# Performance work log

Hardware: AMD Instinct MI355X
Metric: run time of the kernel (lower is better)

Reference implementation:

```python
import jax, jax.numpy as jnp
import numpy as np

B, S, D_IN, D_OUT = 4, 2048, 1024, 64
USE_MASK = True

def setup_inputs() -> dict:
    key = jax.random.key(0)
    ks = jax.random.split(key, 6)
    return {
        "inputs_for_keys": jax.random.normal(ks[0], (B, S, D_IN), jnp.float32),
        "inputs_for_values": jax.random.normal(ks[1], (B, S, D_IN), jnp.float32),
        "inputs_for_queries": jax.random.normal(ks[2], (B, S, D_IN), jnp.float32),
        "Weight_Q": jax.random.normal(ks[3], (D_IN, D_OUT), jnp.float32) * 0.02,
        "Weight_K": jax.random.normal(ks[4], (D_IN, D_OUT), jnp.float32) * 0.02,
        "Weight_V": jax.random.normal(ks[5], (D_IN, D_OUT), jnp.float32) * 0.02,
    }

def reference(inputs_for_keys, inputs_for_values, inputs_for_queries, Weight_Q, Weight_K, Weight_V):
    Q = jnp.einsum('bsd,de->bse', inputs_for_queries, Weight_Q)
    K = jnp.einsum('bsd,de->bse', inputs_for_keys, Weight_K)
    V = jnp.einsum('bsd,de->bse', inputs_for_values, Weight_V)
    # scores: [B, S_q, S_k], scaled by sqrt(d_out)
    scores = jnp.einsum('bqe,bke->bqk', Q, K) / np.sqrt(D_OUT).astype(np.float32)
    if USE_MASK:
        # -inf strictly above the diagonal (causal mask), matching
        # transpose(tril(ones*-inf, -1)) in the original.
        q_idx = jnp.arange(S)[:, None]
        k_idx = jnp.arange(S)[None, :]
        scores = jnp.where(k_idx > q_idx, -jnp.inf, scores)
    attn = jax.nn.softmax(scores, axis=-1)
    return jnp.einsum('bqk,bke->bqe', attn, V)
```

## Files before the change

### kernel.cpp

```cpp
#include <hip/hip_runtime.h>
#include <hip/hip_bf16.h>
#include <stdint.h>

typedef __bf16 bf16_t;
typedef __bf16 bf16x8 __attribute__((ext_vector_type(8)));
typedef float f32x4 __attribute__((ext_vector_type(4)));

#define L2E 1.44269504088896340736f

static __device__ __forceinline__ f32x4 mfma16(bf16x8 a, bf16x8 b, f32x4 c) {
  return __builtin_amdgcn_mfma_f32_16x16x32_bf16(a, b, c, 0, 0, 0);
}

static __device__ __forceinline__ void gload_lds16(const void* g, void* l) {
  __builtin_amdgcn_global_load_lds(
      (const __attribute__((address_space(1))) uint32_t*)g,
      (__attribute__((address_space(3))) uint32_t*)l, 16, 0, 0);
}

__global__ __launch_bounds__(256) void wt_kernel(const float* __restrict__ Wq,
                                                 const float* __restrict__ Wk,
                                                 const float* __restrict__ Wv,
                                                 bf16_t* __restrict__ Wt) {
  int gid = blockIdx.x * 256 + threadIdx.x;
  int proj = gid >> 16;
  int rem = gid & 65535;
  int k = rem >> 6, n = rem & 63;
  const float* W = (proj == 0) ? Wq : (proj == 1) ? Wk : Wv;
  float v = W[rem];
  if (proj == 0) v *= 0.125f;
  Wt[proj * 65536 + n * 1024 + k] = (bf16_t)v;
}

__global__ __launch_bounds__(128) void proj_kernel(
    const float* __restrict__ Xq, const float* __restrict__ Xk, const float* __restrict__ Xv,
    const bf16_t* __restrict__ Wt,
    bf16_t* __restrict__ Qb, bf16_t* __restrict__ Kb, bf16_t* __restrict__ Vt) {
  __shared__ alignas(16) char Wl[2][16384];
  __shared__ bf16_t Vb[2][16][68];

  int tid = threadIdx.x;
  int w = tid >> 6, lane = tid & 63;
  int l15 = lane & 15, g = lane >> 4;
  int bid = blockIdx.x;
  int p = bid >> 8, rt = bid & 255;
  int m0 = rt * 32;
  const float* X = (p == 0) ? Xq : (p == 1) ? Xk : Xv;
  const char* wbase = (const char*)(Wt + (size_t)p * 65536);

  int sn = w * 4 + (lane >> 4);
  int skb = (lane & 15) * 16;

  auto stageW = [&](int c, int buf) {
#pragma unroll
    for (int i = 0; i < 8; ++i) {
      int n = i * 8 + sn;
      const char* src = wbase + (size_t)n * 2048 + c * 256 + (skb ^ ((n & 7) << 4));
      gload_lds16(src, &Wl[buf][i * 2048 + w * 1024]);
    }
  };

  const float* xrow = X + (size_t)(m0 + w * 16 + l15) * 1024 + g * 8;

  auto issueX = [&](int c, float4* xr) {
    const float* b = xrow + c * 128;
#pragma unroll
    for (int j = 0; j < 4; ++j) {
      xr[2 * j] = *(const float4*)(b + j * 32);
      xr[2 * j + 1] = *(const float4*)(b + j * 32 + 4);
    }
  };

  f32x4 acc[4] = {};

  auto compute = [&](int c, const float4* xr) {
    const char* wb = &Wl[c & 1][0];
#pragma unroll
    for (int j = 0; j < 4; ++j) {
      bf16x8 af;
      af[0] = (bf16_t)xr[2 * j].x; af[1] = (bf16_t)xr[2 * j].y;
      af[2] = (bf16_t)xr[2 * j].z; af[3] = (bf16_t)xr[2 * j].w;
      af[4] = (bf16_t)xr[2 * j + 1].x; af[5] = (bf16_t)xr[2 * j + 1].y;
      af[6] = (bf16_t)xr[2 * j + 1].z; af[7] = (bf16_t)xr[2 * j + 1].w;
#pragma unroll
      for (int ct = 0; ct < 4; ++ct) {
        int n = ct * 16 + l15;
        bf16x8 bfr = *(const bf16x8*)(wb + n * 256 + ((j * 64 + g * 16) ^ ((n & 7) << 4)));
        acc[ct] = mfma16(af, bfr, acc[ct]);
      }
    }
  };

  float4 xA[8], xB[8];
  stageW(0, 0);
  issueX(0, xA);
#pragma unroll
  for (int c = 0; c < 8; ++c) {
    __syncthreads();
    if (c < 7) {
      stageW(c + 1, (c + 1) & 1);
      if (c & 1) issueX(c + 1, xA); else issueX(c + 1, xB);
    }
    if (c & 1) compute(c, xB); else compute(c, xA);
  }

  if (p < 2) {
    bf16_t* Ob = (p == 0) ? Qb : Kb;
    size_t rbase = (size_t)(m0 + w * 16 + g * 4) * 64 + l15;
#pragma unroll
    for (int ct = 0; ct < 4; ++ct)
#pragma unroll
      for (int r = 0; r < 4; ++r)
        Ob[rbase + (size_t)r * 64 + ct * 16] = (bf16_t)acc[ct][r];
  } else {
#pragma unroll
    for (int ct = 0; ct < 4; ++ct)
#pragma unroll
      for (int r = 0; r < 4; ++r)
        Vb[w][g * 4 + r][ct * 16 + l15] = (bf16_t)acc[ct][r];
    int d = lane;
    bf16_t tmp[16];
#pragma unroll
    for (int s = 0; s < 16; ++s) tmp[s] = Vb[w][s][d];
    int b = rt >> 6;
    int s0 = (m0 & 2047) + w * 16;
    bf16_t* dst = Vt + ((size_t)(b * 64 + d)) * 2048 + s0;
    *(uint4*)dst = *(const uint4*)&tmp[0];
    *(uint4*)(dst + 8) = *(const uint4*)&tmp[8];
  }
}

#define NW 8
__global__ __launch_bounds__(512) void attn_kernel(
    const bf16_t* __restrict__ Qb, const bf16_t* __restrict__ Kb,
    const bf16_t* __restrict__ Vt, float* __restrict__ Out) {
  __shared__ alignas(16) char Psm[NW * 4096];
  __shared__ float accL[NW][32][64];
  __shared__ float mL[NW][32];
  __shared__ float lL[NW][32];

  int b = blockIdx.y;
  int x = blockIdx.x;
  int qt = (b >= 2) ? (63 - x) : x;
  int q0 = qt * 32;
  int tid = threadIdx.x;
  int w = tid >> 6, lane = tid & 63;
  int l15 = lane & 15, g = lane >> 4;
  char* Pw = Psm + w * 4096;

  bf16x8 qf[2][2];
#pragma unroll
  for (int h = 0; h < 2; ++h) {
    size_t qrow = (size_t)(b * 2048 + q0 + h * 16 + l15) * 64;
    qf[h][0] = *(const bf16x8*)(Qb + qrow + g * 8);
    qf[h][1] = *(const bf16x8*)(Qb + qrow + 32 + g * 8);
  }

  float m_run[2][4], l_run[2][4];
  f32x4 acc_o[2][4] = {};
#pragma unroll
  for (int h = 0; h < 2; ++h)
#pragma unroll
    for (int r = 0; r < 4; ++r) { m_run[h][r] = -1e30f; l_run[h][r] = 0.f; }

  int ntiles = (q0 + 95) >> 6;
  const bf16_t* kbase = Kb + (size_t)b * 2048 * 64;
  const bf16_t* vbase = Vt + (size_t)b * 64 * 2048;

  for (int t = w; t < ntiles; t += NW) {
    int kv0 = t * 64;
    f32x4 s[2][4] = {};
#pragma unroll
    for (int ct = 0; ct < 4; ++ct) {
      const bf16_t* kr = kbase + (size_t)(kv0 + ct * 16 + l15) * 64 + g * 8;
      bf16x8 kf0 = *(const bf16x8*)kr;
      bf16x8 kf1 = *(const bf16x8*)(kr + 32);
#pragma unroll
      for (int h = 0; h < 2; ++h) {
        s[h][ct] = mfma16(qf[h][0], kf0, s[h][ct]);
        s[h][ct] = mfma16(qf[h][1], kf1, s[h][ct]);
      }
    }
    if (t == ntiles - 1) {
#pragma unroll
      for (int h = 0; h < 2; ++h)
#pragma unroll
        for (int ct = 0; ct < 4; ++ct)
#pragma unroll
          for (int r = 0; r < 4; ++r) {
            int kg_ = kv0 + ct * 16 + l15;
            int qg_ = q0 + h * 16 + g * 4 + r;
            if (kg_ > qg_) s[h][ct][r] = -1e30f;
          }
    }

#pragma unroll
    for (int h = 0; h < 2; ++h)
#pragma unroll
      for (int r = 0; r < 4; ++r) {
        float mx = fmaxf(fmaxf(s[h][0][r], s[h][1][r]), fmaxf(s[h][2][r], s[h][3][r]));
        mx = fmaxf(mx, __shfl_xor(mx, 1, 64));
        mx = fmaxf(mx, __shfl_xor(mx, 2, 64));
        mx = fmaxf(mx, __shfl_xor(mx, 4, 64));
        mx = fmaxf(mx, __shfl_xor(mx, 8, 64));
        float mnew = fmaxf(m_run[h][r], mx);
        float scale = exp2f((m_run[h][r] - mnew) * L2E);
        m_run[h][r] = mnew;
        float ps = 0.f;
        int qrl = h * 16 + g * 4 + r;
        char* pb = Pw + qrl * 128;
        int swp = (qrl & 7) << 4;
#pragma unroll
        for (int ct = 0; ct < 4; ++ct) {
          float p = exp2f((s[h][ct][r] - mnew) * L2E);
          ps += p;
          *(bf16_t*)(pb + ((ct * 32 + l15 * 2) ^ swp)) = (bf16_t)p;
        }
        ps += __shfl_xor(ps, 1, 64);
        ps += __shfl_xor(ps, 2, 64);
        ps += __shfl_xor(ps, 4, 64);
        ps += __shfl_xor(ps, 8, 64);
        l_run[h][r] = l_run[h][r] * scale + ps;
#pragma unroll
        for (int dt = 0; dt < 4; ++dt) acc_o[h][dt][r] *= scale;
      }

    int swpr = (l15 & 7) << 4;
#pragma unroll
    for (int ks = 0; ks < 2; ++ks) {
      bf16x8 pf0 = *(const bf16x8*)(Pw + l15 * 128 + ((ks * 64 + g * 16) ^ swpr));
      bf16x8 pf1 = *(const bf16x8*)(Pw + (16 + l15) * 128 + ((ks * 64 + g * 16) ^ swpr));
#pragma unroll
      for (int dt = 0; dt < 4; ++dt) {
        const bf16_t* vr = vbase + (size_t)(dt * 16 + l15) * 2048 + kv0 + ks * 32 + g * 8;
        bf16x8 vf = *(const bf16x8*)vr;
        acc_o[0][dt] = mfma16(pf0, vf, acc_o[0][dt]);
        acc_o[1][dt] = mfma16(pf1, vf, acc_o[1][dt]);
      }
    }
  }

  if (l15 == 0) {
#pragma unroll
    for (int h = 0; h < 2; ++h)
#pragma unroll
      for (int r = 0; r < 4; ++r) {
        mL[w][h * 16 + g * 4 + r] = m_run[h][r];
        lL[w][h * 16 + g * 4 + r] = l_run[h][r];
      }
  }
#pragma unroll
  for (int h = 0; h < 2; ++h)
#pragma unroll
    for (int dt = 0; dt < 4; ++dt)
#pragma unroll
      for (int r = 0; r < 4; ++r)
        accL[w][h * 16 + g * 4 + r][dt * 16 + l15] = acc_o[h][dt][r];
  __syncthreads();

  int row = tid >> 4, c0 = (tid & 15) * 4;
  float M = -1e30f;
#pragma unroll
  for (int w2 = 0; w2 < NW; ++w2) M = fmaxf(M, mL[w2][row]);
  float L = 0.f;
  f32x4 o = {0.f, 0.f, 0.f, 0.f};
#pragma unroll
  for (int w2 = 0; w2 < NW; ++w2) {
    float sc = exp2f((mL[w2][row] - M) * L2E);
    L += lL[w2][row] * sc;
    f32x4 a = *(const f32x4*)&accL[w2][row][c0];
    o[0] += sc * a[0]; o[1] += sc * a[1]; o[2] += sc * a[2]; o[3] += sc * a[3];
  }
  float inv = 1.0f / L;
  float4 o4 = {o[0] * inv, o[1] * inv, o[2] * inv, o[3] * inv};
  *(float4*)&Out[(size_t)(b * 2048 + q0 + row) * 64 + c0] = o4;
}

extern "C" void kernel_launch(void* const* d_in, const int* in_sizes, int n_in,
                              void* d_out, int out_size, void* d_ws, size_t ws_size,
                              hipStream_t stream) {
  const float* Xk = (const float*)d_in[0];
  const float* Xv = (const float*)d_in[1];
  const float* Xq = (const float*)d_in[2];
  const float* Wq = (const float*)d_in[3];
  const float* Wk = (const float*)d_in[4];
  const float* Wv = (const float*)d_in[5];
  float* Out = (float*)d_out;

  bf16_t* ws = (bf16_t*)d_ws;
  bf16_t* Qb = ws;
  bf16_t* Kb = ws + 524288;
  bf16_t* Vt = ws + 1048576;
  bf16_t* Wt = ws + 1572864;

  wt_kernel<<<dim3(768), dim3(256), 0, stream>>>(Wq, Wk, Wv, Wt);
  proj_kernel<<<dim3(768), dim3(128), 0, stream>>>(Xq, Xk, Xv, Wt, Qb, Kb, Vt);
  attn_kernel<<<dim3(64, 4), dim3(512), 0, stream>>>(Qb, Kb, Vt, Out);
}
```

Baseline: 55.84 us.

## Split projection K-dimension across warps with LDS reduction, drop weight LDS staging

The projection kernel now gives each block 16 rows and splits the 1024-wide reduction across four warps. Each warp streams its X slice and reads the bf16 weights straight from global memory with register double-buffering, and the partial sums are reduced through shared memory. This doubles the block count and removes the async LDS staging of the weights, with the aim of more parallelism and latency hiding on the memory-bound projection. In exchange each block re-reads the weights without LDS reuse and pays for an extra reduction and sync.

```diff
diff --git a/kernel.cpp b/kernel.cpp
--- a/kernel.cpp
+++ b/kernel.cpp
@@ -10,12 +10,6 @@
 
 static __device__ __forceinline__ f32x4 mfma16(bf16x8 a, bf16x8 b, f32x4 c) {
   return __builtin_amdgcn_mfma_f32_16x16x32_bf16(a, b, c, 0, 0, 0);
-}
-
-static __device__ __forceinline__ void gload_lds16(const void* g, void* l) {
-  __builtin_amdgcn_global_load_lds(
-      (const __attribute__((address_space(1))) uint32_t*)g,
-      (__attribute__((address_space(3))) uint32_t*)l, 16, 0, 0);
 }
 
 __global__ __launch_bounds__(256) void wt_kernel(const float* __restrict__ Wq,
@@ -32,101 +26,85 @@
   Wt[proj * 65536 + n * 1024 + k] = (bf16_t)v;
 }
 
-__global__ __launch_bounds__(128) void proj_kernel(
+__global__ __launch_bounds__(256, 4) void proj_kernel(
     const float* __restrict__ Xq, const float* __restrict__ Xk, const float* __restrict__ Xv,
     const bf16_t* __restrict__ Wt,
     bf16_t* __restrict__ Qb, bf16_t* __restrict__ Kb, bf16_t* __restrict__ Vt) {
-  __shared__ alignas(16) char Wl[2][16384];
-  __shared__ bf16_t Vb[2][16][68];
+  __shared__ float Msm[4][16][68];
+  __shared__ bf16_t Vsm[16][68];
 
   int tid = threadIdx.x;
   int w = tid >> 6, lane = tid & 63;
   int l15 = lane & 15, g = lane >> 4;
   int bid = blockIdx.x;
-  int p = bid >> 8, rt = bid & 255;
-  int m0 = rt * 32;
+  int p = bid >> 9, t = bid & 511;
+  int m0 = t * 16;
   const float* X = (p == 0) ? Xq : (p == 1) ? Xk : Xv;
-  const char* wbase = (const char*)(Wt + (size_t)p * 65536);
-
-  int sn = w * 4 + (lane >> 4);
-  int skb = (lane & 15) * 16;
-
-  auto stageW = [&](int c, int buf) {
-#pragma unroll
-    for (int i = 0; i < 8; ++i) {
-      int n = i * 8 + sn;
-      const char* src = wbase + (size_t)n * 2048 + c * 256 + (skb ^ ((n & 7) << 4));
-      gload_lds16(src, &Wl[buf][i * 2048 + w * 1024]);
-    }
-  };
-
-  const float* xrow = X + (size_t)(m0 + w * 16 + l15) * 1024 + g * 8;
-
-  auto issueX = [&](int c, float4* xr) {
-    const float* b = xrow + c * 128;
-#pragma unroll
-    for (int j = 0; j < 4; ++j) {
-      xr[2 * j] = *(const float4*)(b + j * 32);
-      xr[2 * j + 1] = *(const float4*)(b + j * 32 + 4);
-    }
-  };
+
+  const float* xk = X + (size_t)(m0 + l15) * 1024 + w * 256 + g * 8;
+  const bf16_t* wrow = Wt + p * 65536 + l15 * 1024 + w * 256 + g * 8;
 
   f32x4 acc[4] = {};
 
-  auto compute = [&](int c, const float4* xr) {
-    const char* wb = &Wl[c & 1][0];
-#pragma unroll
-    for (int j = 0; j < 4; ++j) {
-      bf16x8 af;
-      af[0] = (bf16_t)xr[2 * j].x; af[1] = (bf16_t)xr[2 * j].y;
-      af[2] = (bf16_t)xr[2 * j].z; af[3] = (bf16_t)xr[2 * j].w;
-      af[4] = (bf16_t)xr[2 * j + 1].x; af[5] = (bf16_t)xr[2 * j + 1].y;
-      af[6] = (bf16_t)xr[2 * j + 1].z; af[7] = (bf16_t)xr[2 * j + 1].w;
-#pragma unroll
-      for (int ct = 0; ct < 4; ++ct) {
-        int n = ct * 16 + l15;
-        bf16x8 bfr = *(const bf16x8*)(wb + n * 256 + ((j * 64 + g * 16) ^ ((n & 7) << 4)));
-        acc[ct] = mfma16(af, bfr, acc[ct]);
-      }
-    }
-  };
-
-  float4 xA[8], xB[8];
-  stageW(0, 0);
-  issueX(0, xA);
-#pragma unroll
-  for (int c = 0; c < 8; ++c) {
-    __syncthreads();
-    if (c < 7) {
-      stageW(c + 1, (c + 1) & 1);
-      if (c & 1) issueX(c + 1, xA); else issueX(c + 1, xB);
-    }
-    if (c & 1) compute(c, xB); else compute(c, xA);
+  float4 a0x = *(const float4*)xk;
+  float4 a0y = *(const float4*)(xk + 4);
+  bf16x8 w0[4], w1[4];
+#pragma unroll
+  for (int ct = 0; ct < 4; ++ct) w0[ct] = *(const bf16x8*)(wrow + ct * 16384);
+
+  float4 a1x, a1y;
+#pragma unroll
+  for (int ks = 0; ks < 8; ++ks) {
+    if (ks < 7) {
+      const float* xn = xk + (ks + 1) * 32;
+      a1x = *(const float4*)xn;
+      a1y = *(const float4*)(xn + 4);
+#pragma unroll
+      for (int ct = 0; ct < 4; ++ct)
+        w1[ct] = *(const bf16x8*)(wrow + ct * 16384 + (ks + 1) * 32);
+    }
+    bf16x8 af;
+    af[0] = (bf16_t)a0x.x; af[1] = (bf16_t)a0x.y; af[2] = (bf16_t)a0x.z; af[3] = (bf16_t)a0x.w;
+    af[4] = (bf16_t)a0y.x; af[5] = (bf16_t)a0y.y; af[6] = (bf16_t)a0y.z; af[7] = (bf16_t)a0y.w;
+#pragma unroll
+    for (int ct = 0; ct < 4; ++ct) acc[ct] = mfma16(af, w0[ct], acc[ct]);
+    a0x = a1x; a0y = a1y;
+#pragma unroll
+    for (int ct = 0; ct < 4; ++ct) w0[ct] = w1[ct];
+  }
+
+#pragma unroll
+  for (int ct = 0; ct < 4; ++ct)
+#pragma unroll
+    for (int r = 0; r < 4; ++r)
+      Msm[w][g * 4 + r][ct * 16 + l15] = acc[ct][r];
+  __syncthreads();
+
+  int row = tid >> 4, c0 = (tid & 15) * 4;
+  f32x4 s = *(const f32x4*)&Msm[0][row][c0];
+#pragma unroll
+  for (int w2 = 1; w2 < 4; ++w2) {
+    f32x4 q = *(const f32x4*)&Msm[w2][row][c0];
+    s[0] += q[0]; s[1] += q[1]; s[2] += q[2]; s[3] += q[3];
   }
 
   if (p < 2) {
     bf16_t* Ob = (p == 0) ? Qb : Kb;
-    size_t rbase = (size_t)(m0 + w * 16 + g * 4) * 64 + l15;
-#pragma unroll
-    for (int ct = 0; ct < 4; ++ct)
-#pragma unroll
-      for (int r = 0; r < 4; ++r)
-        Ob[rbase + (size_t)r * 64 + ct * 16] = (bf16_t)acc[ct][r];
+    bf16_t o4[4] = {(bf16_t)s[0], (bf16_t)s[1], (bf16_t)s[2], (bf16_t)s[3]};
+    *(uint2*)&Ob[(size_t)(m0 + row) * 64 + c0] = *(const uint2*)o4;
   } else {
 #pragma unroll
-    for (int ct = 0; ct < 4; ++ct)
-#pragma unroll
-      for (int r = 0; r < 4; ++r)
-        Vb[w][g * 4 + r][ct * 16 + l15] = (bf16_t)acc[ct][r];
-    int d = lane;
-    bf16_t tmp[16];
-#pragma unroll
-    for (int s = 0; s < 16; ++s) tmp[s] = Vb[w][s][d];
-    int b = rt >> 6;
-    int s0 = (m0 & 2047) + w * 16;
-    bf16_t* dst = Vt + ((size_t)(b * 64 + d)) * 2048 + s0;
-    *(uint4*)dst = *(const uint4*)&tmp[0];
-    *(uint4*)(dst + 8) = *(const uint4*)&tmp[8];
+    for (int i = 0; i < 4; ++i) Vsm[row][c0 + i] = (bf16_t)s[i];
+    __syncthreads();
+    if (tid < 128) {
+      int d = tid >> 1, h = tid & 1;
+      int b = t >> 7;
+      int s_ = (t & 127) * 16 + h * 8;
+      bf16_t tmp[8];
+#pragma unroll
+      for (int i = 0; i < 8; ++i) tmp[i] = Vsm[h * 8 + i][d];
+      *(uint4*)(Vt + ((size_t)(b * 64 + d)) * 2048 + s_) = *(const uint4*)tmp;
+    }
   }
 }
 
@@ -294,6 +272,6 @@
   bf16_t* Wt = ws + 1572864;
 
   wt_kernel<<<dim3(768), dim3(256), 0, stream>>>(Wq, Wk, Wv, Wt);
-  proj_kernel<<<dim3(768), dim3(128), 0, stream>>>(Xq, Xk, Xv, Wt, Qb, Kb, Vt);
+  proj_kernel<<<dim3(1536), dim3(256), 0, stream>>>(Xq, Xk, Xv, Wt, Qb, Kb, Vt);
   attn_kernel<<<dim3(64, 4), dim3(512), 0, stream>>>(Qb, Kb, Vt, Out);
 }
```

Measured after the change: 65.63 us. 1.18x slower.

## Restructure projection kernel: full-weight LDS staging, 6 waves per block, 256 blocks

Applied to the files above, without the earlier changes.

The projection kernel now stages the whole 128KB bf16 weight matrix for one projection into LDS once per block. Each of 6 waves computes an independent 16-row tile, streaming X directly from global memory with register double buffering. This removes the per-chunk barriers and double-buffered weight staging. A wave whose tile belongs to a different projection than the staged one reads weights from global memory instead. Outputs are staged through LDS so Q and K can be written with vectorized stores, at the cost of one block per CU and a large up-front LDS fill.

```diff
diff --git a/kernel.cpp b/kernel.cpp
--- a/kernel.cpp
+++ b/kernel.cpp
@@ -32,98 +32,95 @@
   Wt[proj * 65536 + n * 1024 + k] = (bf16_t)v;
 }
 
-__global__ __launch_bounds__(128) void proj_kernel(
+__global__ __launch_bounds__(384, 1) void proj_kernel(
     const float* __restrict__ Xq, const float* __restrict__ Xk, const float* __restrict__ Xv,
     const bf16_t* __restrict__ Wt,
     bf16_t* __restrict__ Qb, bf16_t* __restrict__ Kb, bf16_t* __restrict__ Vt) {
-  __shared__ alignas(16) char Wl[2][16384];
-  __shared__ bf16_t Vb[2][16][68];
+  __shared__ alignas(16) char Wl[131072];
+  __shared__ alignas(16) bf16_t Osm[6][16][72];
 
   int tid = threadIdx.x;
-  int w = tid >> 6, lane = tid & 63;
+  int w = tid / 64, lane = tid & 63;
   int l15 = lane & 15, g = lane >> 4;
   int bid = blockIdx.x;
-  int p = bid >> 8, rt = bid & 255;
-  int m0 = rt * 32;
+
+  int p_lds = (bid * 6 + 2) >> 9;
+
+  {
+    const char* wb = (const char*)(Wt + (size_t)p_lds * 65536);
+    for (int n = w; n < 64; n += 6) {
+#pragma unroll
+      for (int h = 0; h < 2; ++h) {
+        const char* src = wb + n * 2048 + h * 1024 + ((lane * 16) ^ ((n & 7) << 4));
+        gload_lds16(src, Wl + n * 2048 + h * 1024);
+      }
+    }
+  }
+  __syncthreads();
+
+  int T = bid * 6 + w;
+  int p = T >> 9;
+  int t = T & 511;
+  int m0 = t * 16;
   const float* X = (p == 0) ? Xq : (p == 1) ? Xk : Xv;
-  const char* wbase = (const char*)(Wt + (size_t)p * 65536);
-
-  int sn = w * 4 + (lane >> 4);
-  int skb = (lane & 15) * 16;
-
-  auto stageW = [&](int c, int buf) {
-#pragma unroll
-    for (int i = 0; i < 8; ++i) {
-      int n = i * 8 + sn;
-      const char* src = wbase + (size_t)n * 2048 + c * 256 + (skb ^ ((n & 7) << 4));
-      gload_lds16(src, &Wl[buf][i * 2048 + w * 1024]);
-    }
+  const float* xrow = X + (size_t)(m0 + l15) * 1024 + g * 8;
+
+  f32x4 acc[4] = {};
+
+  auto wfrag_lds = [&](int ct, int byteoff) -> bf16x8 {
+    int n = ct * 16 + l15;
+    return *(const bf16x8*)(Wl + n * 2048 + (byteoff ^ ((n & 7) << 4)));
   };
-
-  const float* xrow = X + (size_t)(m0 + w * 16 + l15) * 1024 + g * 8;
-
-  auto issueX = [&](int c, float4* xr) {
-    const float* b = xrow + c * 128;
-#pragma unroll
-    for (int j = 0; j < 4; ++j) {
-      xr[2 * j] = *(const float4*)(b + j * 32);
-      xr[2 * j + 1] = *(const float4*)(b + j * 32 + 4);
-    }
+  auto wfrag_glob = [&](int ct, int byteoff) -> bf16x8 {
+    int n = ct * 16 + l15;
+    return *(const bf16x8*)((const char*)(Wt + (size_t)p * 65536) + n * 2048 + byteoff);
   };
 
-  f32x4 acc[4] = {};
-
-  auto compute = [&](int c, const float4* xr) {
-    const char* wb = &Wl[c & 1][0];
-#pragma unroll
-    for (int j = 0; j < 4; ++j) {
-      bf16x8 af;
-      af[0] = (bf16_t)xr[2 * j].x; af[1] = (bf16_t)xr[2 * j].y;
-      af[2] = (bf16_t)xr[2 * j].z; af[3] = (bf16_t)xr[2 * j].w;
-      af[4] = (bf16_t)xr[2 * j + 1].x; af[5] = (bf16_t)xr[2 * j + 1].y;
-      af[6] = (bf16_t)xr[2 * j + 1].z; af[7] = (bf16_t)xr[2 * j + 1].w;
+  auto run = [&](auto wf) {
+    float4 pa[2][4];
+    auto ld = [&](int j, float4* r) {
+      const float* b = xrow + j * 64;
+      r[0] = *(const float4*)b;        r[1] = *(const float4*)(b + 4);
+      r[2] = *(const float4*)(b + 32); r[3] = *(const float4*)(b + 36);
+    };
+    ld(0, pa[0]);
+#pragma unroll
+    for (int j = 0; j < 16; ++j) {
+      if (j < 15) ld(j + 1, pa[(j + 1) & 1]);
+      float4* r = pa[j & 1];
+      bf16x8 a0, a1;
+      a0[0] = (bf16_t)r[0].x; a0[1] = (bf16_t)r[0].y; a0[2] = (bf16_t)r[0].z; a0[3] = (bf16_t)r[0].w;
+      a0[4] = (bf16_t)r[1].x; a0[5] = (bf16_t)r[1].y; a0[6] = (bf16_t)r[1].z; a0[7] = (bf16_t)r[1].w;
+      a1[0] = (bf16_t)r[2].x; a1[1] = (bf16_t)r[2].y; a1[2] = (bf16_t)r[2].z; a1[3] = (bf16_t)r[2].w;
+      a1[4] = (bf16_t)r[3].x; a1[5] = (bf16_t)r[3].y; a1[6] = (bf16_t)r[3].z; a1[7] = (bf16_t)r[3].w;
 #pragma unroll
       for (int ct = 0; ct < 4; ++ct) {
-        int n = ct * 16 + l15;
-        bf16x8 bfr = *(const bf16x8*)(wb + n * 256 + ((j * 64 + g * 16) ^ ((n & 7) << 4)));
-        acc[ct] = mfma16(af, bfr, acc[ct]);
+        acc[ct] = mfma16(a0, wf(ct, j * 128 + g * 16), acc[ct]);
+        acc[ct] = mfma16(a1, wf(ct, j * 128 + 64 + g * 16), acc[ct]);
       }
     }
   };
-
-  float4 xA[8], xB[8];
-  stageW(0, 0);
-  issueX(0, xA);
-#pragma unroll
-  for (int c = 0; c < 8; ++c) {
-    __syncthreads();
-    if (c < 7) {
-      stageW(c + 1, (c + 1) & 1);
-      if (c & 1) issueX(c + 1, xA); else issueX(c + 1, xB);
-    }
-    if (c & 1) compute(c, xB); else compute(c, xA);
-  }
+  if (p == p_lds) run(wfrag_lds); else run(wfrag_glob);
+
+#pragma unroll
+  for (int ct = 0; ct < 4; ++ct)
+#pragma unroll
+    for (int r = 0; r < 4; ++r)
+      Osm[w][g * 4 + r][ct * 16 + l15] = (bf16_t)acc[ct][r];
 
   if (p < 2) {
     bf16_t* Ob = (p == 0) ? Qb : Kb;
-    size_t rbase = (size_t)(m0 + w * 16 + g * 4) * 64 + l15;
-#pragma unroll
-    for (int ct = 0; ct < 4; ++ct)
-#pragma unroll
-      for (int r = 0; r < 4; ++r)
-        Ob[rbase + (size_t)r * 64 + ct * 16] = (bf16_t)acc[ct][r];
+    int row = lane >> 2, c0 = (lane & 3) * 16;
+    uint4 v0 = *(const uint4*)&Osm[w][row][c0];
+    uint4 v1 = *(const uint4*)&Osm[w][row][c0 + 8];
+    *(uint4*)&Ob[(size_t)(m0 + row) * 64 + c0] = v0;
+    *(uint4*)&Ob[(size_t)(m0 + row) * 64 + c0 + 8] = v1;
   } else {
-#pragma unroll
-    for (int ct = 0; ct < 4; ++ct)
-#pragma unroll
-      for (int r = 0; r < 4; ++r)
-        Vb[w][g * 4 + r][ct * 16 + l15] = (bf16_t)acc[ct][r];
     int d = lane;
     bf16_t tmp[16];
 #pragma unroll
-    for (int s = 0; s < 16; ++s) tmp[s] = Vb[w][s][d];
-    int b = rt >> 6;
-    int s0 = (m0 & 2047) + w * 16;
+    for (int s = 0; s < 16; ++s) tmp[s] = Osm[w][s][d];
+    int b = t >> 7, s0 = (t & 127) * 16;
     bf16_t* dst = Vt + ((size_t)(b * 64 + d)) * 2048 + s0;
     *(uint4*)dst = *(const uint4*)&tmp[0];
     *(uint4*)(dst + 8) = *(const uint4*)&tmp[8];
@@ -294,6 +291,6 @@
   bf16_t* Wt = ws + 1572864;
 
   wt_kernel<<<dim3(768), dim3(256), 0, stream>>>(Wq, Wk, Wv, Wt);
-  proj_kernel<<<dim3(768), dim3(128), 0, stream>>>(Xq, Xk, Xv, Wt, Qb, Kb, Vt);
+  proj_kernel<<<dim3(256), dim3(384), 0, stream>>>(Xq, Xk, Xv, Wt, Qb, Kb, Vt);
   attn_kernel<<<dim3(64, 4), dim3(512), 0, stream>>>(Qb, Kb, Vt, Out);
 }
```

After: 54.05 us. 3.2% less time.
